# Performance work log

Hardware: AMD Instinct MI355X
Metric: run time of the kernel (lower is better)

Reference implementation:

```python
import jax, jax.numpy as jnp
import numpy as np

B, N, K = 8, 8192, 12
C_IN, C_HID, C_OUT = 3, 128, 256


def setup_inputs() -> dict:
    key = jax.random.key(0)
    ks = jax.random.split(key, 10)
    x = jax.random.normal(ks[0], (B, N, C_IN), dtype=jnp.float32)
    knn_idx = jax.random.randint(ks[1], (B, N, K), 0, N, dtype=jnp.int32)
    s1 = 1.0 / np.sqrt(C_IN)
    s2 = 1.0 / np.sqrt(C_HID)
    W1 = jax.random.uniform(ks[2], (C_HID, C_IN), jnp.float32, -s1, s1)
    b1 = jax.random.uniform(ks[3], (C_HID,), jnp.float32, -s1, s1)
    Wc0 = jax.random.uniform(ks[4], (C_HID, C_HID), jnp.float32, -s2, s2)
    bc0 = jax.random.uniform(ks[5], (C_HID,), jnp.float32, -s2, s2)
    Wc1 = jax.random.uniform(ks[6], (C_HID, C_HID), jnp.float32, -s2, s2)
    bc1 = jax.random.uniform(ks[7], (C_HID,), jnp.float32, -s2, s2)
    W2 = jax.random.uniform(ks[8], (C_OUT, C_HID), jnp.float32, -s2, s2)
    b2 = jax.random.uniform(ks[9], (C_OUT,), jnp.float32, -s2, s2)
    return {"x": x, "knn_idx": knn_idx, "W1": W1, "b1": b1,
            "Wc0": Wc0, "bc0": bc0, "Wc1": Wc1, "bc1": bc1,
            "W2": W2, "b2": b2}


def reference(x, knn_idx, W1, b1, Wc0, bc0, Wc1, bc1, W2, b2):
    # knn_group: gather neighbor features -> [B, N, K, C_IN]
    bidx = jnp.arange(x.shape[0])[:, None, None]
    g = x[bidx, knn_idx]                                   # [B,N,K,C]
    # trans1 (Linear)
    h = jnp.einsum('bnkc,hc->bnkh', g, W1) + b1            # [B,N,K,H]
    # two 1x1 Conv2d over channel dim + ReLU (layout transpose is a no-op in math)
    h = jax.nn.relu(jnp.einsum('bnkh,oh->bnko', h, Wc0) + bc0)
    h = jax.nn.relu(jnp.einsum('bnkh,oh->bnko', h, Wc1) + bc1)
    # mean over neighbor (k) dim
    m = jnp.mean(h, axis=2)                                # [B,N,H]
    # trans2 (Linear)
    out = jnp.einsum('bnh,oh->bno', m, W2) + b2            # [B,N,C_OUT]
    return out
```

## Files before the change

kernel.cpp:

```cpp
#include <hip/hip_runtime.h>


typedef __attribute__((ext_vector_type(8))) _Float16 h8;
typedef __attribute__((ext_vector_type(4))) _Float16 h4;
typedef __attribute__((ext_vector_type(4))) float    f4;

#define MFMA_H __builtin_amdgcn_mfma_f32_16x16x32_f16

#define LO_SCALE_INV 2.44140625e-4f

__device__ __forceinline__ void splitW8(const float* __restrict__ p, h8& hi, h8& lo) {
    const float4 a = *(const float4*)p;
    const float4 b = *(const float4*)(p + 4);
    const float v[8] = {a.x, a.y, a.z, a.w, b.x, b.y, b.z, b.w};
#pragma unroll
    for (int j = 0; j < 8; ++j) {
        const _Float16 h = (_Float16)v[j];
        hi[j] = h;
        lo[j] = (_Float16)((v[j] - (float)h) * 4096.f);
    }
}

__global__ __launch_bounds__(256) void k_mlp(
    const float* __restrict__ x,
    const float* __restrict__ W1, const float* __restrict__ b1,
    const float* __restrict__ Wc0, const float* __restrict__ bc0,
    const float* __restrict__ Wc1, const float* __restrict__ bc1,
    _Float16* __restrict__ t)
{
    __shared__ __align__(16) _Float16 hA[64 * 128];
    __shared__ __align__(16) _Float16 hB[64 * 128];

    const int tid = threadIdx.x;
    const int bid = blockIdx.x;
    const int lb  = (bid & 7) * 128 + (bid >> 3);
    const long pblk = (long)lb * 64;

    {
        const int pt  = tid >> 2;
        const int q4  = tid & 3;
        const int ch0 = q4 * 32;
        const float* xp = x + (pblk + pt) * 3;
        const float x0 = xp[0], x1 = xp[1], x2 = xp[2];
        const int p7 = pt & 7;
#pragma unroll
        for (int q = 0; q < 4; ++q) {
            h8 hv;
#pragma unroll
            for (int j = 0; j < 8; ++j) {
                const int c = ch0 + q * 8 + j;
                float v = b1[c];
                v = fmaf(W1[c * 3 + 0], x0, v);
                v = fmaf(W1[c * 3 + 1], x1, v);
                v = fmaf(W1[c * 3 + 2], x2, v);
                hv[j] = (_Float16)v;
            }
            const int chunk = q4 * 4 + q;
            *(h8*)&hA[pt * 128 + ((chunk ^ p7) << 3)] = hv;
        }
    }
    __syncthreads();

    const int lane = tid & 63;
    const int w  = tid >> 6;
    const int fr = lane & 15;
    const int g  = lane >> 4;
    const int ocb = w * 32;

#pragma unroll
    for (int layer = 0; layer < 2; ++layer) {
        const float* W  = layer ? Wc1 : Wc0;
        const float* bp = layer ? bc1 : bc0;

        h8 Ah[2][4], Al[2][4];
#pragma unroll
        for (int T = 0; T < 2; ++T)
#pragma unroll
            for (int c = 0; c < 4; ++c)
                splitW8(W + (long)(ocb + T * 16 + fr) * 128 + c * 32 + g * 8,
                        Ah[T][c], Al[T][c]);

        f4 bias[2];
#pragma unroll
        for (int T = 0; T < 2; ++T) {
            const float4 bv = *(const float4*)(bp + ocb + T * 16 + g * 4);
            bias[T] = (f4){bv.x, bv.y, bv.z, bv.w};
        }

        const _Float16* hin = layer ? hB : hA;
        const f4 zf = {0.f, 0.f, 0.f, 0.f};

#pragma unroll 2
        for (int p = 0; p < 4; ++p) {
            const int pt = p * 16 + fr;
            const int p7 = pt & 7;
            h8 B[4];
#pragma unroll
            for (int c = 0; c < 4; ++c)
                B[c] = *(const h8*)&hin[pt * 128 + (((4 * c + g) ^ p7) << 3)];

            f4 ahi[2] = {bias[0], bias[1]};
            f4 alo[2] = {zf, zf};
#pragma unroll
            for (int c = 0; c < 4; ++c) {
#pragma unroll
                for (int T = 0; T < 2; ++T) {
                    ahi[T] = MFMA_H(Ah[T][c], B[c], ahi[T], 0, 0, 0);
                    alo[T] = MFMA_H(Al[T][c], B[c], alo[T], 0, 0, 0);
                }
            }
#pragma unroll
            for (int T = 0; T < 2; ++T) {
                const int ocoff = ocb + T * 16 + g * 4;
                h4 o;
#pragma unroll
                for (int r = 0; r < 4; ++r)
                    o[r] = (_Float16)fmaxf(fmaf(alo[T][r], LO_SCALE_INV, ahi[T][r]), 0.f);
                if (layer == 0) {
                    const int sidx = pt * 128 + (((ocoff >> 3) ^ p7) << 3) + (ocoff & 7);
                    *(h4*)&hB[sidx] = o;
                } else {
                    *(h4*)&t[(pblk + pt) * 128 + ocoff] = o;
                }
            }
        }
        if (layer == 0) __syncthreads();
    }
}

__global__ __launch_bounds__(256) void k_out2(
    const int* __restrict__ knn,
    const _Float16* __restrict__ t,
    const float* __restrict__ W2, const float* __restrict__ b2,
    float* __restrict__ out)
{
    __shared__ __align__(16) _Float16 mS[128 * 128];

    const int tid = threadIdx.x;
    const int bid = blockIdx.x;
    const int lb  = (bid & 7) * 64 + (bid >> 3);
    const long pbase = (long)lb * 128;
    const long bbase = (pbase >> 13) << 13;

    {
        const int oct = tid & 7;
        const int o8  = oct * 8;
#pragma unroll 1
        for (int pass = 0; pass < 4; ++pass) {
            const int ptl = pass * 32 + (tid >> 3);
            const int* ip = knn + (pbase + ptl) * 12;
            int idx[12];
            *(int4*)&idx[0] = *(const int4*)(ip + 0);
            *(int4*)&idx[4] = *(const int4*)(ip + 4);
            *(int4*)&idx[8] = *(const int4*)(ip + 8);

            float acc[16];
#pragma unroll
            for (int c = 0; c < 16; ++c) acc[c] = 0.f;
#pragma unroll 4
            for (int k = 0; k < 12; ++k) {
                const _Float16* tp = t + (bbase + idx[k]) * 128;
                const h8 va = *(const h8*)(tp + o8);
                const h8 vb = *(const h8*)(tp + 64 + o8);
#pragma unroll
                for (int j = 0; j < 8; ++j) acc[j] += (float)va[j];
#pragma unroll
                for (int j = 0; j < 8; ++j) acc[8 + j] += (float)vb[j];
            }
            h8 oa, ob;
#pragma unroll
            for (int j = 0; j < 8; ++j) {
                oa[j] = (_Float16)(acc[j] * (1.f / 12.f));
                ob[j] = (_Float16)(acc[8 + j] * (1.f / 12.f));
            }
            const int p7 = ptl & 7;
            *(h8*)&mS[ptl * 128 + ((oct ^ p7) << 3)]       = oa;
            *(h8*)&mS[ptl * 128 + (((oct + 8) ^ p7) << 3)] = ob;
        }
    }
    __syncthreads();

    const int lane = tid & 63;
    const int w  = tid >> 6;
    const int fr = lane & 15;
    const int g  = lane >> 4;
    const f4 zf = {0.f, 0.f, 0.f, 0.f};

#pragma unroll 1
    for (int half = 0; half < 2; ++half) {
        const int ocb = half * 128 + w * 32;

        h8 Ah[2][4], Al[2][4];
#pragma unroll
        for (int T = 0; T < 2; ++T)
#pragma unroll
            for (int c = 0; c < 4; ++c)
                splitW8(W2 + (long)(ocb + T * 16 + fr) * 128 + c * 32 + g * 8,
                        Ah[T][c], Al[T][c]);

        f4 bias[2];
#pragma unroll
        for (int T = 0; T < 2; ++T) {
            const float4 bv = *(const float4*)(b2 + ocb + T * 16 + g * 4);
            bias[T] = (f4){bv.x, bv.y, bv.z, bv.w};
        }

#pragma unroll 2
        for (int p = 0; p < 8; ++p) {
            const int ptl = p * 16 + fr;
            const int p7  = ptl & 7;
            h8 B[4];
#pragma unroll
            for (int c = 0; c < 4; ++c)
                B[c] = *(const h8*)&mS[ptl * 128 + (((4 * c + g) ^ p7) << 3)];

            f4 ahi[2] = {bias[0], bias[1]};
            f4 alo[2] = {zf, zf};
#pragma unroll
            for (int c = 0; c < 4; ++c) {
#pragma unroll
                for (int T = 0; T < 2; ++T) {
                    ahi[T] = MFMA_H(Ah[T][c], B[c], ahi[T], 0, 0, 0);
                    alo[T] = MFMA_H(Al[T][c], B[c], alo[T], 0, 0, 0);
                }
            }
#pragma unroll
            for (int T = 0; T < 2; ++T) {
                float4 o;
                o.x = fmaf(alo[T][0], LO_SCALE_INV, ahi[T][0]);
                o.y = fmaf(alo[T][1], LO_SCALE_INV, ahi[T][1]);
                o.z = fmaf(alo[T][2], LO_SCALE_INV, ahi[T][2]);
                o.w = fmaf(alo[T][3], LO_SCALE_INV, ahi[T][3]);
                *(float4*)&out[(pbase + ptl) * 256 + ocb + T * 16 + g * 4] = o;
            }
        }
    }
}


extern "C" void kernel_launch(void* const* d_in, const int* in_sizes, int n_in,
                              void* d_out, int out_size, void* d_ws, size_t ws_size,
                              hipStream_t stream)
{
    const float* x   = (const float*)d_in[0];
    const int*   knn = (const int*)d_in[1];
    const float* W1  = (const float*)d_in[2];
    const float* b1  = (const float*)d_in[3];
    const float* Wc0 = (const float*)d_in[4];
    const float* bc0 = (const float*)d_in[5];
    const float* Wc1 = (const float*)d_in[6];
    const float* bc1 = (const float*)d_in[7];
    const float* W2  = (const float*)d_in[8];
    const float* b2  = (const float*)d_in[9];
    float* out = (float*)d_out;

    _Float16* t = (_Float16*)d_ws;

    k_mlp <<<dim3(1024), dim3(256), 0, stream>>>(x, W1, b1, Wc0, bc0, Wc1, bc1, t);
    k_out2<<<dim3(512),  dim3(256), 0, stream>>>(knn, t, W2, b2, out);
}
```

Baseline: 77.27 us.

## Precompute fp16 hi/lo weight planes once and shrink output blocks to 64 points

Adds a prep kernel that splits Wc0, Wc1 and W2 into fp16 hi and lo planes in workspace, so the MLP and output kernels load prepared halves instead of re-splitting fp32 weights in every block. The output kernel now handles 64 points per block across 1024 blocks, with half the shared memory, and preloads the first weight strip before the gather phase. Output stores become nontemporal. The cost is an extra kernel launch and a dependency on workspace space at a 16MB offset.

```diff
diff --git a/kernel.cpp b/kernel.cpp
--- a/kernel.cpp
+++ b/kernel.cpp
@@ -9,23 +9,92 @@
 
 #define LO_SCALE_INV 2.44140625e-4f
 
-__device__ __forceinline__ void splitW8(const float* __restrict__ p, h8& hi, h8& lo) {
-    const float4 a = *(const float4*)p;
-    const float4 b = *(const float4*)(p + 4);
-    const float v[8] = {a.x, a.y, a.z, a.w, b.x, b.y, b.z, b.w};
-#pragma unroll
-    for (int j = 0; j < 8; ++j) {
-        const _Float16 h = (_Float16)v[j];
-        hi[j] = h;
-        lo[j] = (_Float16)((v[j] - (float)h) * 4096.f);
+#define WC0H 0
+#define WC0L 16384
+#define WC1H 32768
+#define WC1L 49152
+#define W2H  65536
+#define W2L  98304
+
+__global__ void k_prep(const float* __restrict__ Wc0, const float* __restrict__ Wc1,
+                       const float* __restrict__ W2, _Float16* __restrict__ planes)
+{
+    const int i = blockIdx.x * 256 + threadIdx.x;
+    float v; _Float16 *ph, *pl;
+    if (i < 16384) {
+        v = Wc0[i]; ph = planes + WC0H + i; pl = planes + WC0L + i;
+    } else if (i < 32768) {
+        const int j = i - 16384;
+        v = Wc1[j]; ph = planes + WC1H + j; pl = planes + WC1L + j;
+    } else {
+        const int j = i - 32768;
+        v = W2[j];  ph = planes + W2H + j;  pl = planes + W2L + j;
+    }
+    const _Float16 h = (_Float16)v;
+    *ph = h;
+    *pl = (_Float16)((v - (float)h) * 4096.f);
+}
+
+template <class F>
+__device__ __forceinline__ void pass32p(
+    const _Float16* __restrict__ hin,
+    const _Float16* __restrict__ wh,
+    const _Float16* __restrict__ wl,
+    const float* __restrict__ bias,
+    int fr, int g, F&& emit)
+{
+    h8 Ah[2][4], Al[2][4];
+#pragma unroll
+    for (int T = 0; T < 2; ++T)
+#pragma unroll
+        for (int c = 0; c < 4; ++c) {
+            const long off = (long)(T * 16 + fr) * 128 + c * 32 + g * 8;
+            Ah[T][c] = *(const h8*)(wh + off);
+            Al[T][c] = *(const h8*)(wl + off);
+        }
+
+    f4 bv[2] = {{0.f, 0.f, 0.f, 0.f}, {0.f, 0.f, 0.f, 0.f}};
+    if (bias) {
+#pragma unroll
+        for (int T = 0; T < 2; ++T) {
+            const float4 q = *(const float4*)(bias + T * 16 + g * 4);
+            bv[T] = (f4){q.x, q.y, q.z, q.w};
+        }
+    }
+
+#pragma unroll
+    for (int p = 0; p < 4; ++p) {
+        const int pt = p * 16 + fr;
+        const int p7 = pt & 7;
+        h8 B[4];
+#pragma unroll
+        for (int c = 0; c < 4; ++c)
+            B[c] = *(const h8*)&hin[pt * 128 + (((4 * c + g) ^ p7) << 3)];
+
+        f4 ahi[2] = {bv[0], bv[1]};
+        f4 alo[2] = {{0.f, 0.f, 0.f, 0.f}, {0.f, 0.f, 0.f, 0.f}};
+#pragma unroll
+        for (int c = 0; c < 4; ++c)
+#pragma unroll
+            for (int T = 0; T < 2; ++T) {
+                ahi[T] = MFMA_H(Ah[T][c], B[c], ahi[T], 0, 0, 0);
+                alo[T] = MFMA_H(Al[T][c], B[c], alo[T], 0, 0, 0);
+            }
+        f4 rv[2];
+#pragma unroll
+        for (int T = 0; T < 2; ++T)
+#pragma unroll
+            for (int j = 0; j < 4; ++j)
+                rv[T][j] = fmaf(alo[T][j], LO_SCALE_INV, ahi[T][j]);
+        emit(p, rv);
     }
 }
 
 __global__ __launch_bounds__(256) void k_mlp(
     const float* __restrict__ x,
     const float* __restrict__ W1, const float* __restrict__ b1,
-    const float* __restrict__ Wc0, const float* __restrict__ bc0,
-    const float* __restrict__ Wc1, const float* __restrict__ bc1,
+    const float* __restrict__ bc0, const float* __restrict__ bc1,
+    const _Float16* __restrict__ planes,
     _Float16* __restrict__ t)
 {
     __shared__ __align__(16) _Float16 hA[64 * 128];
@@ -66,87 +135,81 @@
     const int fr = lane & 15;
     const int g  = lane >> 4;
     const int ocb = w * 32;
-
-#pragma unroll
-    for (int layer = 0; layer < 2; ++layer) {
-        const float* W  = layer ? Wc1 : Wc0;
-        const float* bp = layer ? bc1 : bc0;
-
-        h8 Ah[2][4], Al[2][4];
-#pragma unroll
-        for (int T = 0; T < 2; ++T)
-#pragma unroll
-            for (int c = 0; c < 4; ++c)
-                splitW8(W + (long)(ocb + T * 16 + fr) * 128 + c * 32 + g * 8,
-                        Ah[T][c], Al[T][c]);
-
-        f4 bias[2];
+    const long strip = (long)ocb * 128;
+
+    auto storeMid = [&](_Float16* hout, int p, f4* rv) {
+        const int pt = p * 16 + fr;
+        const int p7 = pt & 7;
 #pragma unroll
         for (int T = 0; T < 2; ++T) {
-            const float4 bv = *(const float4*)(bp + ocb + T * 16 + g * 4);
-            bias[T] = (f4){bv.x, bv.y, bv.z, bv.w};
-        }
-
-        const _Float16* hin = layer ? hB : hA;
-        const f4 zf = {0.f, 0.f, 0.f, 0.f};
-
-#pragma unroll 2
-        for (int p = 0; p < 4; ++p) {
-            const int pt = p * 16 + fr;
-            const int p7 = pt & 7;
-            h8 B[4];
-#pragma unroll
-            for (int c = 0; c < 4; ++c)
-                B[c] = *(const h8*)&hin[pt * 128 + (((4 * c + g) ^ p7) << 3)];
-
-            f4 ahi[2] = {bias[0], bias[1]};
-            f4 alo[2] = {zf, zf};
-#pragma unroll
-            for (int c = 0; c < 4; ++c) {
+            const int ocoff = ocb + T * 16 + g * 4;
+            h4 o;
+#pragma unroll
+            for (int r = 0; r < 4; ++r) o[r] = (_Float16)fmaxf(rv[T][r], 0.f);
+            const int sidx = pt * 128 + (((ocoff >> 3) ^ p7) << 3) + (ocoff & 7);
+            *(h4*)&hout[sidx] = o;
+        }
+    };
+
+    pass32p(hA, planes + WC0H + strip, planes + WC0L + strip, bc0 + ocb, fr, g,
+            [&](int p, f4* rv) { storeMid(hB, p, rv); });
+    __syncthreads();
+
+    pass32p(hB, planes + WC1H + strip, planes + WC1L + strip, bc1 + ocb, fr, g,
+            [&](int p, f4* rv) {
+                const int ptl = p * 16 + fr;
+                const long pt = pblk + ptl;
 #pragma unroll
                 for (int T = 0; T < 2; ++T) {
-                    ahi[T] = MFMA_H(Ah[T][c], B[c], ahi[T], 0, 0, 0);
-                    alo[T] = MFMA_H(Al[T][c], B[c], alo[T], 0, 0, 0);
+                    const int ocoff = ocb + T * 16 + g * 4;
+                    h4 o;
+#pragma unroll
+                    for (int r = 0; r < 4; ++r)
+                        o[r] = (_Float16)fmaxf(rv[T][r], 0.f);
+                    *(h4*)&t[pt * 128 + ocoff] = o;
                 }
-            }
-#pragma unroll
-            for (int T = 0; T < 2; ++T) {
-                const int ocoff = ocb + T * 16 + g * 4;
-                h4 o;
-#pragma unroll
-                for (int r = 0; r < 4; ++r)
-                    o[r] = (_Float16)fmaxf(fmaf(alo[T][r], LO_SCALE_INV, ahi[T][r]), 0.f);
-                if (layer == 0) {
-                    const int sidx = pt * 128 + (((ocoff >> 3) ^ p7) << 3) + (ocoff & 7);
-                    *(h4*)&hB[sidx] = o;
-                } else {
-                    *(h4*)&t[(pblk + pt) * 128 + ocoff] = o;
-                }
-            }
-        }
-        if (layer == 0) __syncthreads();
-    }
+            });
 }
 
 __global__ __launch_bounds__(256) void k_out2(
     const int* __restrict__ knn,
     const _Float16* __restrict__ t,
-    const float* __restrict__ W2, const float* __restrict__ b2,
+    const _Float16* __restrict__ planes,
+    const float* __restrict__ b2,
     float* __restrict__ out)
 {
-    __shared__ __align__(16) _Float16 mS[128 * 128];
+    __shared__ __align__(16) _Float16 mS[64 * 128];
 
     const int tid = threadIdx.x;
     const int bid = blockIdx.x;
-    const int lb  = (bid & 7) * 64 + (bid >> 3);
-    const long pbase = (long)lb * 128;
+    const int lb  = (bid & 7) * 128 + (bid >> 3);
+    const long pbase = (long)lb * 64;
     const long bbase = (pbase >> 13) << 13;
+
+    const int lane = tid & 63;
+    const int w  = tid >> 6;
+    const int fr = lane & 15;
+    const int g  = lane >> 4;
+
+    auto loadW = [&](int ocb, h8 (&Ah)[2][4], h8 (&Al)[2][4]) {
+#pragma unroll
+        for (int T = 0; T < 2; ++T)
+#pragma unroll
+            for (int c = 0; c < 4; ++c) {
+                const long off = (long)(ocb + T * 16 + fr) * 128 + c * 32 + g * 8;
+                Ah[T][c] = *(const h8*)(planes + W2H + off);
+                Al[T][c] = *(const h8*)(planes + W2L + off);
+            }
+    };
+
+    h8 Ah[2][4], Al[2][4];
+    loadW(0 + w * 32, Ah, Al);
 
     {
         const int oct = tid & 7;
         const int o8  = oct * 8;
 #pragma unroll 1
-        for (int pass = 0; pass < 4; ++pass) {
+        for (int pass = 0; pass < 2; ++pass) {
             const int ptl = pass * 32 + (tid >> 3);
             const int* ip = knn + (pbase + ptl) * 12;
             int idx[12];
@@ -180,33 +243,20 @@
     }
     __syncthreads();
 
-    const int lane = tid & 63;
-    const int w  = tid >> 6;
-    const int fr = lane & 15;
-    const int g  = lane >> 4;
-    const f4 zf = {0.f, 0.f, 0.f, 0.f};
-
 #pragma unroll 1
     for (int half = 0; half < 2; ++half) {
         const int ocb = half * 128 + w * 32;
-
-        h8 Ah[2][4], Al[2][4];
-#pragma unroll
-        for (int T = 0; T < 2; ++T)
-#pragma unroll
-            for (int c = 0; c < 4; ++c)
-                splitW8(W2 + (long)(ocb + T * 16 + fr) * 128 + c * 32 + g * 8,
-                        Ah[T][c], Al[T][c]);
-
-        f4 bias[2];
+        if (half) loadW(ocb, Ah, Al);
+
+        f4 bv[2];
 #pragma unroll
         for (int T = 0; T < 2; ++T) {
-            const float4 bv = *(const float4*)(b2 + ocb + T * 16 + g * 4);
-            bias[T] = (f4){bv.x, bv.y, bv.z, bv.w};
-        }
-
-#pragma unroll 2
-        for (int p = 0; p < 8; ++p) {
+            const float4 q = *(const float4*)(b2 + ocb + T * 16 + g * 4);
+            bv[T] = (f4){q.x, q.y, q.z, q.w};
+        }
+
+#pragma unroll
+        for (int p = 0; p < 4; ++p) {
             const int ptl = p * 16 + fr;
             const int p7  = ptl & 7;
             h8 B[4];
@@ -214,24 +264,23 @@
             for (int c = 0; c < 4; ++c)
                 B[c] = *(const h8*)&mS[ptl * 128 + (((4 * c + g) ^ p7) << 3)];
 
-            f4 ahi[2] = {bias[0], bias[1]};
-            f4 alo[2] = {zf, zf};
-#pragma unroll
-            for (int c = 0; c < 4; ++c) {
+            f4 ahi[2] = {bv[0], bv[1]};
+            f4 alo[2] = {{0.f, 0.f, 0.f, 0.f}, {0.f, 0.f, 0.f, 0.f}};
+#pragma unroll
+            for (int c = 0; c < 4; ++c)
 #pragma unroll
                 for (int T = 0; T < 2; ++T) {
                     ahi[T] = MFMA_H(Ah[T][c], B[c], ahi[T], 0, 0, 0);
                     alo[T] = MFMA_H(Al[T][c], B[c], alo[T], 0, 0, 0);
                 }
-            }
 #pragma unroll
             for (int T = 0; T < 2; ++T) {
-                float4 o;
-                o.x = fmaf(alo[T][0], LO_SCALE_INV, ahi[T][0]);
-                o.y = fmaf(alo[T][1], LO_SCALE_INV, ahi[T][1]);
-                o.z = fmaf(alo[T][2], LO_SCALE_INV, ahi[T][2]);
-                o.w = fmaf(alo[T][3], LO_SCALE_INV, ahi[T][3]);
-                *(float4*)&out[(pbase + ptl) * 256 + ocb + T * 16 + g * 4] = o;
+                f4 o;
+#pragma unroll
+                for (int j = 0; j < 4; ++j)
+                    o[j] = fmaf(alo[T][j], LO_SCALE_INV, ahi[T][j]);
+                float* op = out + (pbase + ptl) * 256 + ocb + T * 16 + g * 4;
+                __builtin_nontemporal_store(o, (f4*)op);
             }
         }
     }
@@ -254,8 +303,10 @@
     const float* b2  = (const float*)d_in[9];
     float* out = (float*)d_out;
 
-    _Float16* t = (_Float16*)d_ws;
-
-    k_mlp <<<dim3(1024), dim3(256), 0, stream>>>(x, W1, b1, Wc0, bc0, Wc1, bc1, t);
-    k_out2<<<dim3(512),  dim3(256), 0, stream>>>(knn, t, W2, b2, out);
-}
+    _Float16* t      = (_Float16*)d_ws;
+    _Float16* planes = (_Float16*)((char*)d_ws + (size_t)16 * 1024 * 1024);
+
+    k_prep<<<dim3(256),  dim3(256), 0, stream>>>(Wc0, Wc1, W2, planes);
+    k_mlp <<<dim3(1024), dim3(256), 0, stream>>>(x, W1, b1, bc0, bc1, planes, t);
+    k_out2<<<dim3(1024), dim3(256), 0, stream>>>(knn, t, planes, b2, out);
+}
```

Result: slower. 87.47 us (+13.2%).

## Gather neighbor means directly into MFMA B-fragment registers, drop shared staging

Applied to the files above, without the earlier changes.

The output kernel no longer gathers neighbor features into a 32 KB shared-memory tile and syncs. Instead each lane accumulates the mean straight into the register layout the MFMA B operand expects, and each wave computes all 256 output channels for its own 32 points. This removes the LDS traffic and the barrier, and may raise occupancy. In exchange every wave now loads and splits the full W2 matrix (4x more weight loads per block), and register pressure rises from holding 64 float accumulators.

```diff
diff --git a/kernel.cpp b/kernel.cpp
--- a/kernel.cpp
+++ b/kernel.cpp
@@ -128,67 +128,65 @@
     }
 }
 
-__global__ __launch_bounds__(256) void k_out2(
+__global__ __launch_bounds__(256) void k_out_s(
     const int* __restrict__ knn,
     const _Float16* __restrict__ t,
     const float* __restrict__ W2, const float* __restrict__ b2,
     float* __restrict__ out)
 {
-    __shared__ __align__(16) _Float16 mS[128 * 128];
-
     const int tid = threadIdx.x;
     const int bid = blockIdx.x;
     const int lb  = (bid & 7) * 64 + (bid >> 3);
     const long pbase = (long)lb * 128;
-    const long bbase = (pbase >> 13) << 13;
-
-    {
-        const int oct = tid & 7;
-        const int o8  = oct * 8;
-#pragma unroll 1
-        for (int pass = 0; pass < 4; ++pass) {
-            const int ptl = pass * 32 + (tid >> 3);
-            const int* ip = knn + (pbase + ptl) * 12;
-            int idx[12];
-            *(int4*)&idx[0] = *(const int4*)(ip + 0);
-            *(int4*)&idx[4] = *(const int4*)(ip + 4);
-            *(int4*)&idx[8] = *(const int4*)(ip + 8);
-
-            float acc[16];
-#pragma unroll
-            for (int c = 0; c < 16; ++c) acc[c] = 0.f;
-#pragma unroll 4
-            for (int k = 0; k < 12; ++k) {
-                const _Float16* tp = t + (bbase + idx[k]) * 128;
-                const h8 va = *(const h8*)(tp + o8);
-                const h8 vb = *(const h8*)(tp + 64 + o8);
-#pragma unroll
-                for (int j = 0; j < 8; ++j) acc[j] += (float)va[j];
-#pragma unroll
-                for (int j = 0; j < 8; ++j) acc[8 + j] += (float)vb[j];
-            }
-            h8 oa, ob;
-#pragma unroll
-            for (int j = 0; j < 8; ++j) {
-                oa[j] = (_Float16)(acc[j] * (1.f / 12.f));
-                ob[j] = (_Float16)(acc[8 + j] * (1.f / 12.f));
-            }
-            const int p7 = ptl & 7;
-            *(h8*)&mS[ptl * 128 + ((oct ^ p7) << 3)]       = oa;
-            *(h8*)&mS[ptl * 128 + (((oct + 8) ^ p7) << 3)] = ob;
-        }
-    }
-    __syncthreads();
+    const long bbase = (long)(bid & 7) * 8192;
 
     const int lane = tid & 63;
     const int w  = tid >> 6;
     const int fr = lane & 15;
     const int g  = lane >> 4;
-    const f4 zf = {0.f, 0.f, 0.f, 0.f};
+    const long base = pbase + w * 32;
+
+    int idx[2][12];
+#pragma unroll
+    for (int p2 = 0; p2 < 2; ++p2) {
+        const int* ip = knn + (base + p2 * 16 + fr) * 12;
+        *(int4*)&idx[p2][0] = *(const int4*)(ip + 0);
+        *(int4*)&idx[p2][4] = *(const int4*)(ip + 4);
+        *(int4*)&idx[p2][8] = *(const int4*)(ip + 8);
+    }
+
+    float acc[2][32];
+#pragma unroll
+    for (int p2 = 0; p2 < 2; ++p2)
+#pragma unroll
+        for (int c = 0; c < 32; ++c) acc[p2][c] = 0.f;
+
+#pragma unroll
+    for (int p2 = 0; p2 < 2; ++p2) {
+#pragma unroll
+        for (int k = 0; k < 12; ++k) {
+            const _Float16* tp = t + (bbase + idx[p2][k]) * 128 + g * 8;
+#pragma unroll
+            for (int c = 0; c < 4; ++c) {
+                const h8 v = *(const h8*)(tp + c * 32);
+#pragma unroll
+                for (int j = 0; j < 8; ++j) acc[p2][c * 8 + j] += (float)v[j];
+            }
+        }
+    }
+
+    h8 B[2][4];
+#pragma unroll
+    for (int p2 = 0; p2 < 2; ++p2)
+#pragma unroll
+        for (int c = 0; c < 4; ++c)
+#pragma unroll
+            for (int j = 0; j < 8; ++j)
+                B[p2][c][j] = (_Float16)(acc[p2][c * 8 + j] * (1.f / 12.f));
 
 #pragma unroll 1
-    for (int half = 0; half < 2; ++half) {
-        const int ocb = half * 128 + w * 32;
+    for (int st = 0; st < 8; ++st) {
+        const int ocb = st * 32;
 
         h8 Ah[2][4], Al[2][4];
 #pragma unroll
@@ -198,32 +196,24 @@
                 splitW8(W2 + (long)(ocb + T * 16 + fr) * 128 + c * 32 + g * 8,
                         Ah[T][c], Al[T][c]);
 
-        f4 bias[2];
+        f4 bv[2];
 #pragma unroll
         for (int T = 0; T < 2; ++T) {
-            const float4 bv = *(const float4*)(b2 + ocb + T * 16 + g * 4);
-            bias[T] = (f4){bv.x, bv.y, bv.z, bv.w};
-        }
-
-#pragma unroll 2
-        for (int p = 0; p < 8; ++p) {
-            const int ptl = p * 16 + fr;
-            const int p7  = ptl & 7;
-            h8 B[4];
-#pragma unroll
-            for (int c = 0; c < 4; ++c)
-                B[c] = *(const h8*)&mS[ptl * 128 + (((4 * c + g) ^ p7) << 3)];
-
-            f4 ahi[2] = {bias[0], bias[1]};
-            f4 alo[2] = {zf, zf};
-#pragma unroll
-            for (int c = 0; c < 4; ++c) {
+            const float4 q = *(const float4*)(b2 + ocb + T * 16 + g * 4);
+            bv[T] = (f4){q.x, q.y, q.z, q.w};
+        }
+
+#pragma unroll
+        for (int p2 = 0; p2 < 2; ++p2) {
+            f4 ahi[2] = {bv[0], bv[1]};
+            f4 alo[2] = {{0.f, 0.f, 0.f, 0.f}, {0.f, 0.f, 0.f, 0.f}};
+#pragma unroll
+            for (int c = 0; c < 4; ++c)
 #pragma unroll
                 for (int T = 0; T < 2; ++T) {
-                    ahi[T] = MFMA_H(Ah[T][c], B[c], ahi[T], 0, 0, 0);
-                    alo[T] = MFMA_H(Al[T][c], B[c], alo[T], 0, 0, 0);
+                    ahi[T] = MFMA_H(Ah[T][c], B[p2][c], ahi[T], 0, 0, 0);
+                    alo[T] = MFMA_H(Al[T][c], B[p2][c], alo[T], 0, 0, 0);
                 }
-            }
 #pragma unroll
             for (int T = 0; T < 2; ++T) {
                 float4 o;
@@ -231,7 +221,7 @@
                 o.y = fmaf(alo[T][1], LO_SCALE_INV, ahi[T][1]);
                 o.z = fmaf(alo[T][2], LO_SCALE_INV, ahi[T][2]);
                 o.w = fmaf(alo[T][3], LO_SCALE_INV, ahi[T][3]);
-                *(float4*)&out[(pbase + ptl) * 256 + ocb + T * 16 + g * 4] = o;
+                *(float4*)&out[(base + p2 * 16 + fr) * 256 + ocb + T * 16 + g * 4] = o;
             }
         }
     }
@@ -256,6 +246,6 @@
 
     _Float16* t = (_Float16*)d_ws;
 
-    k_mlp <<<dim3(1024), dim3(256), 0, stream>>>(x, W1, b1, Wc0, bc0, Wc1, bc1, t);
-    k_out2<<<dim3(512),  dim3(256), 0, stream>>>(knn, t, W2, b2, out);
-}
+    k_mlp  <<<dim3(1024), dim3(256), 0, stream>>>(x, W1, b1, Wc0, bc0, Wc1, bc1, t);
+    k_out_s<<<dim3(512),  dim3(256), 0, stream>>>(knn, t, W2, b2, out);
+}
```

After: 103.0 us. 1.33x slower.

## Fuse MLP and gather-output kernels into one cooperative kernel with grid sync

Applied to the files above, without the earlier changes.

Merges the two kernels into a single cooperative launch of 512 blocks. Each block first runs the per-point MLP on two 64-point chunks, then a grid-wide barrier separates that from the neighbour gather, mean and output projection. This removes the second kernel launch and the gap between launches, and reuses one shared-memory buffer for both phases. The cost is a grid barrier with fence, fewer MLP blocks each doing twice the work, and reliance on all 512 blocks being co-resident (launch bounds ask for 2 blocks per CU). If the cooperative launch fails, it falls back to two separate launches.

```diff
diff --git a/kernel.cpp b/kernel.cpp
--- a/kernel.cpp
+++ b/kernel.cpp
@@ -1,4 +1,7 @@
 #include <hip/hip_runtime.h>
+#include <hip/hip_cooperative_groups.h>
+
+namespace cg = cooperative_groups;
 
 
 typedef __attribute__((ext_vector_type(8))) _Float16 h8;
@@ -21,126 +24,122 @@
     }
 }
 
-__global__ __launch_bounds__(256) void k_mlp(
+__device__ __forceinline__ void mlp_phase(
+    int bid, int tid, _Float16* __restrict__ hA, _Float16* __restrict__ hB,
     const float* __restrict__ x,
     const float* __restrict__ W1, const float* __restrict__ b1,
     const float* __restrict__ Wc0, const float* __restrict__ bc0,
     const float* __restrict__ Wc1, const float* __restrict__ bc1,
     _Float16* __restrict__ t)
 {
-    __shared__ __align__(16) _Float16 hA[64 * 128];
-    __shared__ __align__(16) _Float16 hB[64 * 128];
-
-    const int tid = threadIdx.x;
-    const int bid = blockIdx.x;
-    const int lb  = (bid & 7) * 128 + (bid >> 3);
-    const long pblk = (long)lb * 64;
-
-    {
-        const int pt  = tid >> 2;
-        const int q4  = tid & 3;
-        const int ch0 = q4 * 32;
-        const float* xp = x + (pblk + pt) * 3;
-        const float x0 = xp[0], x1 = xp[1], x2 = xp[2];
-        const int p7 = pt & 7;
-#pragma unroll
-        for (int q = 0; q < 4; ++q) {
-            h8 hv;
-#pragma unroll
-            for (int j = 0; j < 8; ++j) {
-                const int c = ch0 + q * 8 + j;
-                float v = b1[c];
-                v = fmaf(W1[c * 3 + 0], x0, v);
-                v = fmaf(W1[c * 3 + 1], x1, v);
-                v = fmaf(W1[c * 3 + 2], x2, v);
-                hv[j] = (_Float16)v;
-            }
-            const int chunk = q4 * 4 + q;
-            *(h8*)&hA[pt * 128 + ((chunk ^ p7) << 3)] = hv;
-        }
-    }
-    __syncthreads();
-
     const int lane = tid & 63;
     const int w  = tid >> 6;
     const int fr = lane & 15;
     const int g  = lane >> 4;
     const int ocb = w * 32;
 
-#pragma unroll
-    for (int layer = 0; layer < 2; ++layer) {
-        const float* W  = layer ? Wc1 : Wc0;
-        const float* bp = layer ? bc1 : bc0;
-
-        h8 Ah[2][4], Al[2][4];
-#pragma unroll
-        for (int T = 0; T < 2; ++T)
-#pragma unroll
-            for (int c = 0; c < 4; ++c)
-                splitW8(W + (long)(ocb + T * 16 + fr) * 128 + c * 32 + g * 8,
-                        Ah[T][c], Al[T][c]);
-
-        f4 bias[2];
-#pragma unroll
-        for (int T = 0; T < 2; ++T) {
-            const float4 bv = *(const float4*)(bp + ocb + T * 16 + g * 4);
-            bias[T] = (f4){bv.x, bv.y, bv.z, bv.w};
-        }
-
-        const _Float16* hin = layer ? hB : hA;
-        const f4 zf = {0.f, 0.f, 0.f, 0.f};
+#pragma unroll 1
+    for (int qc = 0; qc < 2; ++qc) {
+        const int lb1 = (bid & 7) * 128 + (bid >> 3) * 2 + qc;
+        const long pblk = (long)lb1 * 64;
+
+        {
+            const int pt  = tid >> 2;
+            const int q4  = tid & 3;
+            const int ch0 = q4 * 32;
+            const float* xp = x + (pblk + pt) * 3;
+            const float x0 = xp[0], x1 = xp[1], x2 = xp[2];
+            const int p7 = pt & 7;
+#pragma unroll
+            for (int q = 0; q < 4; ++q) {
+                h8 hv;
+#pragma unroll
+                for (int j = 0; j < 8; ++j) {
+                    const int c = ch0 + q * 8 + j;
+                    float v = b1[c];
+                    v = fmaf(W1[c * 3 + 0], x0, v);
+                    v = fmaf(W1[c * 3 + 1], x1, v);
+                    v = fmaf(W1[c * 3 + 2], x2, v);
+                    hv[j] = (_Float16)v;
+                }
+                const int chunk = q4 * 4 + q;
+                *(h8*)&hA[pt * 128 + ((chunk ^ p7) << 3)] = hv;
+            }
+        }
+        __syncthreads();
+
+#pragma unroll 1
+        for (int layer = 0; layer < 2; ++layer) {
+            const float* W  = layer ? Wc1 : Wc0;
+            const float* bp = layer ? bc1 : bc0;
+
+            h8 Ah[2][4], Al[2][4];
+#pragma unroll
+            for (int T = 0; T < 2; ++T)
+#pragma unroll
+                for (int c = 0; c < 4; ++c)
+                    splitW8(W + (long)(ocb + T * 16 + fr) * 128 + c * 32 + g * 8,
+                            Ah[T][c], Al[T][c]);
+
+            f4 bias[2];
+#pragma unroll
+            for (int T = 0; T < 2; ++T) {
+                const float4 bv = *(const float4*)(bp + ocb + T * 16 + g * 4);
+                bias[T] = (f4){bv.x, bv.y, bv.z, bv.w};
+            }
+
+            const _Float16* hin = layer ? hB : hA;
+            const f4 zf = {0.f, 0.f, 0.f, 0.f};
 
 #pragma unroll 2
-        for (int p = 0; p < 4; ++p) {
-            const int pt = p * 16 + fr;
-            const int p7 = pt & 7;
-            h8 B[4];
-#pragma unroll
-            for (int c = 0; c < 4; ++c)
-                B[c] = *(const h8*)&hin[pt * 128 + (((4 * c + g) ^ p7) << 3)];
-
-            f4 ahi[2] = {bias[0], bias[1]};
-            f4 alo[2] = {zf, zf};
-#pragma unroll
-            for (int c = 0; c < 4; ++c) {
+            for (int p = 0; p < 4; ++p) {
+                const int pt = p * 16 + fr;
+                const int p7 = pt & 7;
+                h8 B[4];
+#pragma unroll
+                for (int c = 0; c < 4; ++c)
+                    B[c] = *(const h8*)&hin[pt * 128 + (((4 * c + g) ^ p7) << 3)];
+
+                f4 ahi[2] = {bias[0], bias[1]};
+                f4 alo[2] = {zf, zf};
+#pragma unroll
+                for (int c = 0; c < 4; ++c) {
+#pragma unroll
+                    for (int T = 0; T < 2; ++T) {
+                        ahi[T] = MFMA_H(Ah[T][c], B[c], ahi[T], 0, 0, 0);
+                        alo[T] = MFMA_H(Al[T][c], B[c], alo[T], 0, 0, 0);
+                    }
+                }
 #pragma unroll
                 for (int T = 0; T < 2; ++T) {
-                    ahi[T] = MFMA_H(Ah[T][c], B[c], ahi[T], 0, 0, 0);
-                    alo[T] = MFMA_H(Al[T][c], B[c], alo[T], 0, 0, 0);
+                    const int ocoff = ocb + T * 16 + g * 4;
+                    h4 o;
+#pragma unroll
+                    for (int r = 0; r < 4; ++r)
+                        o[r] = (_Float16)fmaxf(fmaf(alo[T][r], LO_SCALE_INV, ahi[T][r]), 0.f);
+                    if (layer == 0) {
+                        const int sidx = pt * 128 + (((ocoff >> 3) ^ p7) << 3) + (ocoff & 7);
+                        *(h4*)&hB[sidx] = o;
+                    } else {
+                        *(h4*)&t[(pblk + pt) * 128 + ocoff] = o;
+                    }
                 }
             }
-#pragma unroll
-            for (int T = 0; T < 2; ++T) {
-                const int ocoff = ocb + T * 16 + g * 4;
-                h4 o;
-#pragma unroll
-                for (int r = 0; r < 4; ++r)
-                    o[r] = (_Float16)fmaxf(fmaf(alo[T][r], LO_SCALE_INV, ahi[T][r]), 0.f);
-                if (layer == 0) {
-                    const int sidx = pt * 128 + (((ocoff >> 3) ^ p7) << 3) + (ocoff & 7);
-                    *(h4*)&hB[sidx] = o;
-                } else {
-                    *(h4*)&t[(pblk + pt) * 128 + ocoff] = o;
-                }
-            }
-        }
-        if (layer == 0) __syncthreads();
-    }
-}
-
-__global__ __launch_bounds__(256) void k_out2(
+            if (layer == 0) __syncthreads();
+        }
+    }
+}
+
+__device__ __forceinline__ void out_phase(
+    int bid, int tid, _Float16* __restrict__ mS,
     const int* __restrict__ knn,
     const _Float16* __restrict__ t,
     const float* __restrict__ W2, const float* __restrict__ b2,
     float* __restrict__ out)
 {
-    __shared__ __align__(16) _Float16 mS[128 * 128];
-
-    const int tid = threadIdx.x;
-    const int bid = blockIdx.x;
     const int lb  = (bid & 7) * 64 + (bid >> 3);
     const long pbase = (long)lb * 128;
-    const long bbase = (pbase >> 13) << 13;
+    const long bbase = (long)(bid & 7) * 8192;
 
     {
         const int oct = tid & 7;
@@ -217,13 +216,12 @@
             f4 ahi[2] = {bias[0], bias[1]};
             f4 alo[2] = {zf, zf};
 #pragma unroll
-            for (int c = 0; c < 4; ++c) {
+            for (int c = 0; c < 4; ++c)
 #pragma unroll
                 for (int T = 0; T < 2; ++T) {
                     ahi[T] = MFMA_H(Ah[T][c], B[c], ahi[T], 0, 0, 0);
                     alo[T] = MFMA_H(Al[T][c], B[c], alo[T], 0, 0, 0);
                 }
-            }
 #pragma unroll
             for (int T = 0; T < 2; ++T) {
                 float4 o;
@@ -235,6 +233,48 @@
             }
         }
     }
+}
+
+__global__ __launch_bounds__(256, 2) void k_fused(
+    const float* __restrict__ x, const int* __restrict__ knn,
+    const float* __restrict__ W1, const float* __restrict__ b1,
+    const float* __restrict__ Wc0, const float* __restrict__ bc0,
+    const float* __restrict__ Wc1, const float* __restrict__ bc1,
+    const float* __restrict__ W2, const float* __restrict__ b2,
+    _Float16* __restrict__ t, float* __restrict__ out)
+{
+    __shared__ __align__(16) _Float16 smem[16384];
+
+    const int tid = threadIdx.x;
+    const int bid = blockIdx.x;
+
+    mlp_phase(bid, tid, smem, smem + 8192, x, W1, b1, Wc0, bc0, Wc1, bc1, t);
+
+    __threadfence();
+    cg::this_grid().sync();
+
+    out_phase(bid, tid, smem, knn, t, W2, b2, out);
+}
+
+__global__ __launch_bounds__(256) void k_mlp_fb(
+    const float* __restrict__ x,
+    const float* __restrict__ W1, const float* __restrict__ b1,
+    const float* __restrict__ Wc0, const float* __restrict__ bc0,
+    const float* __restrict__ Wc1, const float* __restrict__ bc1,
+    _Float16* __restrict__ t)
+{
+    __shared__ __align__(16) _Float16 smem[16384];
+    mlp_phase(blockIdx.x, threadIdx.x, smem, smem + 8192,
+              x, W1, b1, Wc0, bc0, Wc1, bc1, t);
+}
+
+__global__ __launch_bounds__(256) void k_out_fb(
+    const int* __restrict__ knn, const _Float16* __restrict__ t,
+    const float* __restrict__ W2, const float* __restrict__ b2,
+    float* __restrict__ out)
+{
+    __shared__ __align__(16) _Float16 smem[16384];
+    out_phase(blockIdx.x, threadIdx.x, smem, knn, t, W2, b2, out);
 }
 
 
@@ -256,6 +296,15 @@
 
     _Float16* t = (_Float16*)d_ws;
 
-    k_mlp <<<dim3(1024), dim3(256), 0, stream>>>(x, W1, b1, Wc0, bc0, Wc1, bc1, t);
-    k_out2<<<dim3(512),  dim3(256), 0, stream>>>(knn, t, W2, b2, out);
-}
+    void* args[] = {
+        (void*)&x, (void*)&knn, (void*)&W1, (void*)&b1, (void*)&Wc0, (void*)&bc0,
+        (void*)&Wc1, (void*)&bc1, (void*)&W2, (void*)&b2, (void*)&t, (void*)&out
+    };
+    const hipError_t e = hipLaunchCooperativeKernel(
+        (const void*)k_fused, dim3(512), dim3(256), args, 0, stream);
+
+    if (e != hipSuccess) {
+        k_mlp_fb<<<dim3(512), dim3(256), 0, stream>>>(x, W1, b1, Wc0, bc0, Wc1, bc1, t);
+        k_out_fb<<<dim3(512), dim3(256), 0, stream>>>(knn, t, W2, b2, out);
+    }
+}
```

After: 206.8 us. 2.68x slower.
